# Performance work log

Hardware: AMD Instinct MI355X
Metric: run time of the kernel (lower is better)

Reference implementation:

```python
import jax, jax.numpy as jnp
import numpy as np

N, H, E, D, L = 100000, 20000, 1600000, 64, 3
F = 4 * D  # ffn hidden = out_dim * 4


def _ln(x, g, b, eps=1e-5):
    mu = x.mean(-1, keepdims=True)
    var = ((x - mu) ** 2).mean(-1, keepdims=True)
    return (x - mu) * jax.lax.rsqrt(var + eps) * g + b


def _gconv(x, W, b, src, dst, inv_sqrt_src, inv_sqrt_dst, n_dst):
    # DGL GraphConv, norm='both': D_dst^{-1/2} A D_src^{-1/2} (x W) + b
    h = (x * inv_sqrt_src[:, None]) @ W
    agg = jax.ops.segment_sum(h[src], dst, num_segments=n_dst)
    return agg * inv_sqrt_dst[:, None] + b


def setup_inputs() -> dict:
    key = jax.random.key(0)
    ks = jax.random.split(key, 24)
    s = 0.05
    inp = {
        'node_features': jax.random.normal(ks[0], (N, D), jnp.float32),
        'edge_src': jax.random.randint(ks[1], (E,), 0, N),
        'edge_dst': jax.random.randint(ks[2], (E,), 0, H),
        'n_hyper': H,
        # stacked per-layer params [L, ...]
        'Wn2h': jax.random.normal(ks[3], (L, D, D), jnp.float32) * s,
        'bn2h': jnp.zeros((L, D), jnp.float32),
        'Wh2n': jax.random.normal(ks[4], (L, D, D), jnp.float32) * s,
        'bh2n': jnp.zeros((L, D), jnp.float32),
        'W1': jax.random.normal(ks[5], (L, D, F), jnp.float32) * s,
        'b1': jnp.zeros((L, F), jnp.float32),
        'W2': jax.random.normal(ks[6], (L, F, D), jnp.float32) * s,
        'b2': jnp.zeros((L, D), jnp.float32),
        'g1': jnp.ones((L, D), jnp.float32),
        'be1': jnp.zeros((L, D), jnp.float32),
        'g2': jnp.ones((L, D), jnp.float32),
        'be2': jnp.zeros((L, D), jnp.float32),
        'gF': jnp.ones((D,), jnp.float32),
        'bF': jnp.zeros((D,), jnp.float32),
        'Wo': jax.random.normal(ks[7], (D, D), jnp.float32) * s,
        'bo': jnp.zeros((D,), jnp.float32),
    }
    return inp


def reference(node_features, edge_src, edge_dst, n_hyper, Wn2h, bn2h, Wh2n, bh2n,
              W1, b1, W2, b2, g1, be1, g2, be2, gF, bF, Wo, bo):
    n_nodes = node_features.shape[0]
    ones = jnp.ones(edge_src.shape[0], node_features.dtype)
    deg_node = jnp.clip(jax.ops.segment_sum(ones, edge_src, num_segments=n_nodes), 1.0)
    deg_hyp = jnp.clip(jax.ops.segment_sum(ones, edge_dst, num_segments=n_hyper), 1.0)
    is_node = jax.lax.rsqrt(deg_node)  # node out-degree^{-1/2}
    is_hyp = jax.lax.rsqrt(deg_hyp)    # hyperedge in-degree^{-1/2}

    def step(h, p):
        Wa, ba, Wb, bb, w1, c1, w2, c2, gg1, ee1, gg2, ee2 = p
        # node -> hyperedge conv (unused attention output is overwritten in the original)
        h_hyper = _gconv(h, Wa, ba, edge_src, edge_dst, is_node, is_hyp, n_hyper)
        # hyperedge -> node conv on reversed graph (degrees swap roles)
        h_node = _gconv(h_hyper, Wb, bb, edge_dst, edge_src, is_hyp, is_node, n_nodes)
        h = _ln(h + h_node, gg1, ee1)
        h_ffn = jax.nn.relu(h @ w1 + c1) @ w2 + c2
        h = _ln(h + h_ffn, gg2, ee2)
        return h, None

    h, _ = jax.lax.scan(step, node_features,
                        (Wn2h, bn2h, Wh2n, bh2n, W1, b1, W2, b2, g1, be1, g2, be2))
    h = _ln(h, gF, bF)
    return h @ Wo + bo
```

## Files before the change

kernel.cpp:

```cpp
#include <hip/hip_runtime.h>

#define HYP 20000
#define NLAYER 3
#define NB_H 313
#define NB_N 391
#define PT 4096

typedef __attribute__((ext_vector_type(8))) short short8;
typedef __attribute__((ext_vector_type(4))) float floatx4;

static __device__ __forceinline__ unsigned short f2bf(float f){
  union { float f; unsigned u; } v; v.f = f;
  unsigned r = v.u + 0x7FFF + ((v.u >> 16) & 1);
  return (unsigned short)(r >> 16);
}

__global__ __launch_bounds__(256) void k_hist(const int* __restrict__ src,
    const int* __restrict__ dst, int E, int* __restrict__ bh, int* __restrict__ bn){
  __shared__ int lh[NB_H + NB_N];
  int tid = threadIdx.x;
  for (int i = tid; i < NB_H + NB_N; i += 256) lh[i] = 0;
  __syncthreads();
  for (int i = blockIdx.x*256 + tid; i < E; i += gridDim.x*256){
    atomicAdd(&lh[dst[i] >> 6], 1);
    atomicAdd(&lh[NB_H + (src[i] >> 8)], 1);
  }
  __syncthreads();
  for (int i = tid; i < NB_H; i += 256) if (lh[i]) atomicAdd(&bh[i], lh[i]);
  for (int i = tid; i < NB_N; i += 256) if (lh[NB_H+i]) atomicAdd(&bn[i], lh[NB_H+i]);
}

__global__ __launch_bounds__(256) void k_bscan(const int* __restrict__ bh,
    const int* __restrict__ bn, int* __restrict__ bstart_h, int* __restrict__ gcur_h,
    int* __restrict__ bstart_n, int* __restrict__ gcur_n){
  __shared__ int ssc[4];
  __shared__ int scarry;
  int tid = threadIdx.x, lane = tid & 63, wv = tid >> 6;
  if (tid == 0) scarry = 0;
  __syncthreads();
  for (int base = 0; base < NB_H; base += 256){
    int i = base + tid; int v = (i < NB_H) ? bh[i] : 0; int x = v;
    #pragma unroll
    for (int o = 1; o < 64; o <<= 1){ int t = __shfl_up(x,o,64); if (lane >= o) x += t; }
    if (lane == 63) ssc[wv] = x;
    __syncthreads();
    int add = (wv>0?ssc[0]:0)+(wv>1?ssc[1]:0)+(wv>2?ssc[2]:0);
    int c = scarry;
    if (i < NB_H){ int ex = c + add + x - v; bstart_h[i] = ex; gcur_h[i] = ex; }
    __syncthreads();
    if (tid == 255) scarry = c + ssc[0]+ssc[1]+ssc[2]+ssc[3];
    __syncthreads();
  }
  if (tid == 0){ bstart_h[NB_H] = scarry; scarry = 0; }
  __syncthreads();
  for (int base = 0; base < NB_N; base += 256){
    int i = base + tid; int v = (i < NB_N) ? bn[i] : 0; int x = v;
    #pragma unroll
    for (int o = 1; o < 64; o <<= 1){ int t = __shfl_up(x,o,64); if (lane >= o) x += t; }
    if (lane == 63) ssc[wv] = x;
    __syncthreads();
    int add = (wv>0?ssc[0]:0)+(wv>1?ssc[1]:0)+(wv>2?ssc[2]:0);
    int c = scarry;
    if (i < NB_N){ int ex = c + add + x - v; bstart_n[i] = ex; gcur_n[i] = ex; }
    __syncthreads();
    if (tid == 255) scarry = c + ssc[0]+ssc[1]+ssc[2]+ssc[3];
    __syncthreads();
  }
  if (tid == 0) bstart_n[NB_N] = scarry;
}

__global__ __launch_bounds__(256) void k_partition(const int* __restrict__ keys,
    const int* __restrict__ pays, int E, int keyshift, int nb,
    int* __restrict__ gcur, unsigned* __restrict__ Ebuf){
  __shared__ unsigned sst[PT];
  __shared__ int lh[NB_N], lpre[NB_N], gb[NB_N];
  __shared__ int ssc[4];
  __shared__ int scarry;
  int tid = threadIdx.x, lane = tid & 63, wv = tid >> 6;
  int base = blockIdx.x*PT;
  int m = min(PT, E - base);
  for (int i = tid; i < nb; i += 256) lh[i] = 0;
  if (tid == 0) scarry = 0;
  __syncthreads();
  unsigned en[16]; int rk[16];
  #pragma unroll
  for (int j = 0; j < 16; ++j){
    int i = base + j*256 + tid;
    if (i < E){
      unsigned k = (unsigned)keys[i], p = (unsigned)pays[i];
      en[j] = (k << keyshift) | p;
      rk[j] = atomicAdd(&lh[en[j] >> 23], 1);
    } else { en[j] = 0; rk[j] = -1; }
  }
  __syncthreads();
  for (int b2 = 0; b2 < nb; b2 += 256){
    int i = b2 + tid; int v = (i < nb) ? lh[i] : 0; int x = v;
    #pragma unroll
    for (int o = 1; o < 64; o <<= 1){ int t = __shfl_up(x,o,64); if (lane >= o) x += t; }
    if (lane == 63) ssc[wv] = x;
    __syncthreads();
    int add = (wv>0?ssc[0]:0)+(wv>1?ssc[1]:0)+(wv>2?ssc[2]:0);
    int c = scarry;
    if (i < nb) lpre[i] = c + add + x - v;
    __syncthreads();
    if (tid == 255) scarry = c + ssc[0]+ssc[1]+ssc[2]+ssc[3];
    __syncthreads();
  }
  for (int i = tid; i < nb; i += 256) gb[i] = atomicAdd(&gcur[i], lh[i]);
  #pragma unroll
  for (int j = 0; j < 16; ++j){
    if (rk[j] >= 0){
      int bk = en[j] >> 23;
      sst[lpre[bk] + rk[j]] = en[j];
    }
  }
  __syncthreads();
  for (int j = tid; j < m; j += 256){
    unsigned e = sst[j];
    int bk = e >> 23;
    Ebuf[gb[bk] + (j - lpre[bk])] = e;
  }
}

__global__ __launch_bounds__(256) void k_build(const unsigned* __restrict__ Ebuf,
    const int* __restrict__ bstart, int keyshift, int ipb, int paymask, int limit,
    int* __restrict__ off, float* __restrict__ isv, int* __restrict__ csr){
  __shared__ int lcnt[256], lpre2[256], lcur[256];
  int tid = threadIdx.x, lane = tid & 63, wv = tid >> 6;
  int b = blockIdx.x;
  int base = bstart[b], m = bstart[b+1] - base;
  for (int i = tid; i < ipb; i += 256) lcnt[i] = 0;
  __syncthreads();
  for (int i = tid; i < m; i += 256){
    unsigned e = Ebuf[base + i];
    atomicAdd(&lcnt[(e >> keyshift) & (ipb-1)], 1);
  }
  __syncthreads();
  if (wv == 0){
    int carry = 0;
    for (int c = 0; c < ipb; c += 64){
      int li = c + lane;
      int v = lcnt[li]; int x = v;
      #pragma unroll
      for (int o = 1; o < 64; o <<= 1){ int t = __shfl_up(x,o,64); if (lane >= o) x += t; }
      int ex = carry + x - v;
      int id = b*ipb + li;
      if (id <= limit) off[id] = base + ex;
      if (id < limit) isv[id] = rsqrtf((float)(v > 0 ? v : 1));
      lpre2[li] = ex;
      carry += __shfl(x, 63, 64);
    }
  }
  for (int i = tid; i < ipb; i += 256) lcur[i] = 0;
  __syncthreads();
  for (int i = tid; i < m; i += 256){
    unsigned e = Ebuf[base + i];
    int li = (e >> keyshift) & (ipb-1);
    int pos = base + lpre2[li] + atomicAdd(&lcur[li], 1);
    csr[pos] = (int)(e & (unsigned)paymask);
  }
}

__global__ void k_prescale(const float* __restrict__ x, const float* __restrict__ isn,
                           unsigned short* __restrict__ xb, int nrows){
  int i = blockIdx.x*blockDim.x + threadIdx.x;
  int st = gridDim.x*blockDim.x;
  int tot = nrows*8;
  for (; i < tot; i += st){
    float s = isn[i >> 3];
    float4 v0 = *(const float4*)&x[(size_t)i*8];
    float4 v1 = *(const float4*)&x[(size_t)i*8 + 4];
    uint4 o;
    o.x = (unsigned)f2bf(v0.x*s) | ((unsigned)f2bf(v0.y*s) << 16);
    o.y = (unsigned)f2bf(v0.z*s) | ((unsigned)f2bf(v0.w*s) << 16);
    o.z = (unsigned)f2bf(v1.x*s) | ((unsigned)f2bf(v1.y*s) << 16);
    o.w = (unsigned)f2bf(v1.z*s) | ((unsigned)f2bf(v1.w*s) << 16);
    *(uint4*)&xb[(size_t)i*8] = o;
  }
}

__global__ void k_cvtall(const float* __restrict__ W1, const float* __restrict__ W2,
                         const float* __restrict__ Wa, const float* __restrict__ Wb,
                         const float* __restrict__ Wo,
                         unsigned short* __restrict__ W1T, unsigned short* __restrict__ W2T,
                         unsigned short* __restrict__ WaT, unsigned short* __restrict__ WbT,
                         unsigned short* __restrict__ WoT){
  int st = gridDim.x*blockDim.x;
  int t0 = blockIdx.x*blockDim.x + threadIdx.x;
  for (int j = t0; j < NLAYER*16384; j += st){
    int l = j >> 14, n = (j >> 6) & 255, k = j & 63;
    W1T[j] = f2bf(W1[l*16384 + k*256 + n]);
  }
  for (int j = t0; j < NLAYER*16384; j += st){
    int l = j >> 14, o = (j >> 8) & 63, kk = j & 255;
    W2T[j] = f2bf(W2[l*16384 + kk*64 + o]);
  }
  for (int j = t0; j < NLAYER*4096; j += st){
    int l = j >> 12, n = (j >> 6) & 63, k = j & 63;
    WaT[j] = f2bf(Wa[l*4096 + k*64 + n]);
  }
  for (int j = t0; j < NLAYER*4096; j += st){
    int l = j >> 12, n = (j >> 6) & 63, k = j & 63;
    WbT[j] = f2bf(Wb[l*4096 + k*64 + n]);
  }
  for (int j = t0; j < 4096; j += st){
    int n = (j >> 6) & 63, k = j & 63;
    WoT[j] = f2bf(Wo[k*64 + n]);
  }
}

template<int LSTR>
static __device__ __forceinline__ void stage64(const unsigned short* __restrict__ gsrc,
    unsigned short* __restrict__ ldst, int tid, int rows){
  int nch = rows*8;
  for (int idx = tid; idx < nch; idx += 256){
    int row = idx >> 3, kc = (idx & 7)*8;
    uint4 v = *(const uint4*)&gsrc[row*64 + kc];
    *(uint4*)&ldst[row*LSTR + kc] = v;
  }
}

static __device__ __forceinline__ void stage_swz(const unsigned short* __restrict__ g,
    int gs, unsigned short* __restrict__ l, int tid){
  #pragma unroll
  for (int it = 0; it < 2; ++it){
    int c = it*256 + tid;
    int row = c >> 3, s = c & 7;
    uint4 v = *(const uint4*)&g[row*gs + s*8];
    *(uint4*)&l[(row << 6) + ((((unsigned)(s ^ row)) & 7u) << 3)] = v;
  }
}

static __device__ __forceinline__ short8 rdswz(const unsigned short* __restrict__ l,
    int row, int slot){
  return *(const short8*)&l[(row << 6) + ((((unsigned)(slot ^ row)) & 7u) << 3)];
}

#define ACC8(u) \
  a0 += __uint_as_float(u.x << 16); a1 += __uint_as_float(u.x & 0xFFFF0000u); \
  a2 += __uint_as_float(u.y << 16); a3 += __uint_as_float(u.y & 0xFFFF0000u); \
  a4 += __uint_as_float(u.z << 16); a5 += __uint_as_float(u.z & 0xFFFF0000u); \
  a6 += __uint_as_float(u.w << 16); a7 += __uint_as_float(u.w & 0xFFFF0000u);

__global__ __launch_bounds__(256) void k_gather8(const unsigned short* __restrict__ feat,
    const int* __restrict__ csr, const int* __restrict__ off,
    unsigned short* __restrict__ agg, int nrows){
  int lane = threadIdx.x & 63, wvi = threadIdx.x >> 6;
  int g = lane >> 3;
  int ch = (lane & 7) * 8;
  int r = blockIdx.x*4 + wvi, stride = gridDim.x*4;
  for (; r < nrows; r += stride){
    int b = off[r], e = off[r+1];
    float a0=0,a1=0,a2=0,a3=0,a4=0,a5=0,a6=0,a7=0;
    int t = b;
    for (; t + 32 <= e; t += 32){
      int s0 = csr[t + g];
      int s1 = csr[t + 8 + g];
      int s2 = csr[t + 16 + g];
      int s3 = csr[t + 24 + g];
      uint4 u0 = *(const uint4*)&feat[(size_t)s0*64 + ch];
      uint4 u1 = *(const uint4*)&feat[(size_t)s1*64 + ch];
      uint4 u2 = *(const uint4*)&feat[(size_t)s2*64 + ch];
      uint4 u3 = *(const uint4*)&feat[(size_t)s3*64 + ch];
      ACC8(u0); ACC8(u1); ACC8(u2); ACC8(u3);
    }
    for (; t + 16 <= e; t += 16){
      int s0 = csr[t + g];
      int s1 = csr[t + 8 + g];
      uint4 u0 = *(const uint4*)&feat[(size_t)s0*64 + ch];
      uint4 u1 = *(const uint4*)&feat[(size_t)s1*64 + ch];
      ACC8(u0); ACC8(u1);
    }
    for (; t < e; t += 8){
      int idx = t + g;
      bool valid = idx < e;
      int s = csr[valid ? idx : b];
      uint4 u = *(const uint4*)&feat[(size_t)s*64 + ch];
      if (!valid){ u.x = 0; u.y = 0; u.z = 0; u.w = 0; }
      ACC8(u);
    }
    #pragma unroll
    for (int o = 8; o <= 32; o <<= 1){
      a0 += __shfl_xor(a0,o,64); a1 += __shfl_xor(a1,o,64);
      a2 += __shfl_xor(a2,o,64); a3 += __shfl_xor(a3,o,64);
      a4 += __shfl_xor(a4,o,64); a5 += __shfl_xor(a5,o,64);
      a6 += __shfl_xor(a6,o,64); a7 += __shfl_xor(a7,o,64);
    }
    if (g == 0){
      uint4 w;
      w.x = (unsigned)f2bf(a0) | ((unsigned)f2bf(a1) << 16);
      w.y = (unsigned)f2bf(a2) | ((unsigned)f2bf(a3) << 16);
      w.z = (unsigned)f2bf(a4) | ((unsigned)f2bf(a5) << 16);
      w.w = (unsigned)f2bf(a6) | ((unsigned)f2bf(a7) << 16);
      *(uint4*)&agg[(size_t)r*64 + ch] = w;
    }
  }
}

__global__ __launch_bounds__(64) void k_mmA(const unsigned short* __restrict__ aggb,
    const unsigned short* __restrict__ WaT, const float* __restrict__ bias,
    const float* __restrict__ ihy, unsigned short* __restrict__ ouths, int nrows){
  __shared__ unsigned short sWb[64*72];
  int lane = threadIdx.x;
  int quad = lane >> 4, n16 = lane & 15;
  for (int idx = lane; idx < 512; idx += 64){
    int row = idx >> 3, kc = (idx & 7)*8;
    *(uint4*)&sWb[row*72 + kc] = *(const uint4*)&WaT[row*64 + kc];
  }
  __syncthreads();
  int rowbase = blockIdx.x*16;
  int arow = min(rowbase + n16, nrows-1);
  short8 a0 = *(const short8*)&aggb[(size_t)arow*64 + quad*8];
  short8 a1 = *(const short8*)&aggb[(size_t)arow*64 + 32 + quad*8];
  float ih[4];
  #pragma unroll
  for (int r = 0; r < 4; ++r) ih[r] = ihy[min(rowbase + quad*4 + r, nrows-1)];
  #pragma unroll
  for (int ot = 0; ot < 4; ++ot){
    floatx4 c = (floatx4){0.f,0.f,0.f,0.f};
    short8 b0 = *(const short8*)&sWb[(ot*16+n16)*72 + quad*8];
    short8 b1 = *(const short8*)&sWb[(ot*16+n16)*72 + 32 + quad*8];
    c = __builtin_amdgcn_mfma_f32_16x16x32_bf16(a0, b0, c, 0, 0, 0);
    c = __builtin_amdgcn_mfma_f32_16x16x32_bf16(a1, b1, c, 0, 0, 0);
    float bl = bias[ot*16 + n16];
    #pragma unroll
    for (int r = 0; r < 4; ++r){
      int rr = rowbase + quad*4 + r;
      if (rr < nrows)
        ouths[(size_t)rr*64 + ot*16 + n16] = f2bf(fmaf(c[r], ih[r], bl) * ih[r]);
    }
  }
}

__global__ __launch_bounds__(256, 6) void k_fused(
    const unsigned short* __restrict__ aggb,
    const unsigned short* __restrict__ WbT,
    const float* __restrict__ bbg,
    const float* __restrict__ isn,
    const float* __restrict__ hin,
    const float* __restrict__ g1v, const float* __restrict__ be1v,
    const unsigned short* __restrict__ W1T, const float* __restrict__ b1g,
    const unsigned short* __restrict__ W2T, const float* __restrict__ b2g,
    const float* __restrict__ g2v, const float* __restrict__ be2v,
    float* __restrict__ Outp, unsigned short* __restrict__ Qs, int nrows)
{
  __shared__ unsigned short sA[64*64];
  __shared__ unsigned short sB[64*64];
  __shared__ unsigned short sPH[4*16*72];
  int tid = threadIdx.x;
  int lane = tid & 63, w = tid >> 6;
  int quad = lane >> 4, n16 = lane & 15;
  int rb = blockIdx.x*64 + w*16;

  stage_swz(WbT, 64, sA, tid);
  __syncthreads();

  float pP[4][4];
  float isr[4];
  {
    int arow = min(rb + n16, nrows-1);
    short8 a0 = *(const short8*)&aggb[(size_t)arow*64 + quad*8];
    short8 a1 = *(const short8*)&aggb[(size_t)arow*64 + 32 + quad*8];
    #pragma unroll
    for (int r = 0; r < 4; ++r) isr[r] = isn[min(rb + quad*4 + r, nrows-1)];
    #pragma unroll
    for (int ot = 0; ot < 4; ++ot){
      floatx4 c = (floatx4){0.f,0.f,0.f,0.f};
      short8 b0 = rdswz(sA, ot*16+n16, quad);
      short8 b1 = rdswz(sA, ot*16+n16, 4+quad);
      c = __builtin_amdgcn_mfma_f32_16x16x32_bf16(a0, b0, c, 0, 0, 0);
      c = __builtin_amdgcn_mfma_f32_16x16x32_bf16(a1, b1, c, 0, 0, 0);
      float bb = bbg[ot*16 + n16];
      #pragma unroll
      for (int r = 0; r < 4; ++r){
        int rr = min(rb + quad*4 + r, nrows-1);
        pP[ot][r] = fmaf(c[r], isr[r], bb) + hin[(size_t)rr*64 + ot*16 + n16];
      }
    }
  }
  {
    float gl[4], bl[4];
    #pragma unroll
    for (int ot = 0; ot < 4; ++ot){ gl[ot] = g1v[ot*16+n16]; bl[ot] = be1v[ot*16+n16]; }
    #pragma unroll
    for (int r = 0; r < 4; ++r){
      float sv = (pP[0][r] + pP[1][r]) + (pP[2][r] + pP[3][r]);
      float q = fmaf(pP[0][r], pP[0][r], pP[1][r]*pP[1][r]) +
                fmaf(pP[2][r], pP[2][r], pP[3][r]*pP[3][r]);
      #pragma unroll
      for (int o = 8; o >= 1; o >>= 1){
        sv += __shfl_xor(sv, o, 64);
        q  += __shfl_xor(q, o, 64);
      }
      float mu = sv*(1.f/64.f);
      float var = fmaf(-mu, mu, q*(1.f/64.f));
      float rs = rsqrtf(var + 1e-5f);
      #pragma unroll
      for (int ot = 0; ot < 4; ++ot)
        pP[ot][r] = fmaf((pP[ot][r]-mu)*rs, gl[ot], bl[ot]);
    }
  }
  unsigned short* myP = &sPH[w*16*72];
  #pragma unroll
  for (int ot = 0; ot < 4; ++ot)
    #pragma unroll
    for (int r = 0; r < 4; ++r)
      myP[(quad*4 + r)*72 + ot*16 + n16] = f2bf(pP[ot][r]);
  short8 p0 = *(const short8*)&myP[n16*72 + quad*8];
  short8 p1 = *(const short8*)&myP[n16*72 + 32 + quad*8];

  floatx4 acc2[4];
  #pragma unroll
  for (int t = 0; t < 4; ++t) acc2[t] = (floatx4){0.f,0.f,0.f,0.f};
  unsigned short* myHc = myP;

  for (int q = 0; q < 4; ++q){
    __syncthreads();
    stage_swz(W1T + q*64*64, 64, sA, tid);
    stage_swz(W2T + q*64, 256, sB, tid);
    __syncthreads();

    #pragma unroll
    for (int ck2 = 0; ck2 < 2; ++ck2){
      #pragma unroll
      for (int nt = 0; nt < 2; ++nt){
        int nl = ck2*32 + nt*16 + n16;
        floatx4 c = (floatx4){0.f,0.f,0.f,0.f};
        short8 b0 = rdswz(sA, nl, quad);
        short8 b1f = rdswz(sA, nl, 4+quad);
        c = __builtin_amdgcn_mfma_f32_16x16x32_bf16(p0, b0, c, 0, 0, 0);
        c = __builtin_amdgcn_mfma_f32_16x16x32_bf16(p1, b1f, c, 0, 0, 0);
        float bb = b1g[q*64 + nl];
        #pragma unroll
        for (int r = 0; r < 4; ++r){
          float h = fmaxf(c[r] + bb, 0.f);
          myHc[(quad*4 + r)*40 + nt*16 + n16] = f2bf(h);
        }
      }
      short8 a2 = *(const short8*)&myHc[n16*40 + quad*8];
      #pragma unroll
      for (int ot = 0; ot < 4; ++ot){
        short8 b2f = rdswz(sB, ot*16+n16, ck2*4 + quad);
        acc2[ot] = __builtin_amdgcn_mfma_f32_16x16x32_bf16(a2, b2f, acc2[ot], 0, 0, 0);
      }
    }
  }

  {
    float gl[4], bel[4];
    #pragma unroll
    for (int ot = 0; ot < 4; ++ot){ gl[ot] = g2v[ot*16 + n16]; bel[ot] = be2v[ot*16 + n16]; }
    float pre[4][4];
    #pragma unroll
    for (int ot = 0; ot < 4; ++ot){
      float b2c = b2g[ot*16 + n16];
      #pragma unroll
      for (int r = 0; r < 4; ++r)
        pre[ot][r] = acc2[ot][r] + b2c + pP[ot][r];
    }
    #pragma unroll
    for (int r = 0; r < 4; ++r){
      float sv = (pre[0][r] + pre[1][r]) + (pre[2][r] + pre[3][r]);
      float q = fmaf(pre[0][r], pre[0][r], pre[1][r]*pre[1][r]) +
                fmaf(pre[2][r], pre[2][r], pre[3][r]*pre[3][r]);
      #pragma unroll
      for (int o = 8; o >= 1; o >>= 1){
        sv += __shfl_xor(sv, o, 64);
        q  += __shfl_xor(q, o, 64);
      }
      float mu = sv*(1.f/64.f);
      float var = fmaf(-mu, mu, q*(1.f/64.f));
      float rs = rsqrtf(var + 1e-5f);
      int rr = rb + quad*4 + r;
      if (rr < nrows){
        float isr2 = isn[rr];
        #pragma unroll
        for (int ot = 0; ot < 4; ++ot){
          float ov = fmaf((pre[ot][r]-mu)*rs, gl[ot], bel[ot]);
          Outp[(size_t)rr*64 + ot*16 + n16] = ov;
          Qs[(size_t)rr*64 + ot*16 + n16] = f2bf(ov * isr2);
        }
      }
    }
  }
}

__global__ __launch_bounds__(256) void k_final(const float* __restrict__ Q,
    const unsigned short* __restrict__ WoT, const float* __restrict__ bog,
    const float* __restrict__ gF, const float* __restrict__ bF,
    float* __restrict__ out, int nrows){
  __shared__ unsigned short sWb[64*72];
  int tid = threadIdx.x;
  int lane = tid & 63, w = tid >> 6;
  int quad = lane >> 4, n16 = lane & 15;
  stage64<72>(WoT, sWb, tid, 64);
  __syncthreads();
  int rowbase = blockIdx.x*64 + w*16;
  int arow = min(rowbase + n16, nrows-1);
  float4 q0 = *(const float4*)&Q[(size_t)arow*64 + quad*8];
  float4 q1 = *(const float4*)&Q[(size_t)arow*64 + quad*8 + 4];
  float4 q2 = *(const float4*)&Q[(size_t)arow*64 + 32 + quad*8];
  float4 q3 = *(const float4*)&Q[(size_t)arow*64 + 32 + quad*8 + 4];
  float s = (q0.x+q0.y+q0.z+q0.w) + (q1.x+q1.y+q1.z+q1.w)
          + (q2.x+q2.y+q2.z+q2.w) + (q3.x+q3.y+q3.z+q3.w);
  float qq = (q0.x*q0.x+q0.y*q0.y+q0.z*q0.z+q0.w*q0.w)
           + (q1.x*q1.x+q1.y*q1.y+q1.z*q1.z+q1.w*q1.w)
           + (q2.x*q2.x+q2.y*q2.y+q2.z*q2.z+q2.w*q2.w)
           + (q3.x*q3.x+q3.y*q3.y+q3.z*q3.z+q3.w*q3.w);
  s += __shfl_xor(s, 16, 64);  qq += __shfl_xor(qq, 16, 64);
  s += __shfl_xor(s, 32, 64);  qq += __shfl_xor(qq, 32, 64);
  float mu = s*(1.f/64.f);
  float var = fmaf(-mu, mu, qq*(1.f/64.f));
  float rs = rsqrtf(var + 1e-5f);
  float4 g0 = *(const float4*)&gF[quad*8];
  float4 g1 = *(const float4*)&gF[quad*8 + 4];
  float4 g2 = *(const float4*)&gF[32 + quad*8];
  float4 g3 = *(const float4*)&gF[32 + quad*8 + 4];
  float4 f0 = *(const float4*)&bF[quad*8];
  float4 f1 = *(const float4*)&bF[quad*8 + 4];
  float4 f2 = *(const float4*)&bF[32 + quad*8];
  float4 f3 = *(const float4*)&bF[32 + quad*8 + 4];
  short8 a0, a1;
  a0[0]=f2bf(fmaf((q0.x-mu)*rs, g0.x, f0.x)); a0[1]=f2bf(fmaf((q0.y-mu)*rs, g0.y, f0.y));
  a0[2]=f2bf(fmaf((q0.z-mu)*rs, g0.z, f0.z)); a0[3]=f2bf(fmaf((q0.w-mu)*rs, g0.w, f0.w));
  a0[4]=f2bf(fmaf((q1.x-mu)*rs, g1.x, f1.x)); a0[5]=f2bf(fmaf((q1.y-mu)*rs, g1.y, f1.y));
  a0[6]=f2bf(fmaf((q1.z-mu)*rs, g1.z, f1.z)); a0[7]=f2bf(fmaf((q1.w-mu)*rs, g1.w, f1.w));
  a1[0]=f2bf(fmaf((q2.x-mu)*rs, g2.x, f2.x)); a1[1]=f2bf(fmaf((q2.y-mu)*rs, g2.y, f2.y));
  a1[2]=f2bf(fmaf((q2.z-mu)*rs, g2.z, f2.z)); a1[3]=f2bf(fmaf((q2.w-mu)*rs, g2.w, f2.w));
  a1[4]=f2bf(fmaf((q3.x-mu)*rs, g3.x, f3.x)); a1[5]=f2bf(fmaf((q3.y-mu)*rs, g3.y, f3.y));
  a1[6]=f2bf(fmaf((q3.z-mu)*rs, g3.z, f3.z)); a1[7]=f2bf(fmaf((q3.w-mu)*rs, g3.w, f3.w));
  #pragma unroll
  for (int ot = 0; ot < 4; ++ot){
    floatx4 c = (floatx4){0.f,0.f,0.f,0.f};
    short8 b0 = *(const short8*)&sWb[(ot*16+n16)*72 + quad*8];
    short8 b1 = *(const short8*)&sWb[(ot*16+n16)*72 + 32 + quad*8];
    c = __builtin_amdgcn_mfma_f32_16x16x32_bf16(a0, b0, c, 0, 0, 0);
    c = __builtin_amdgcn_mfma_f32_16x16x32_bf16(a1, b1, c, 0, 0, 0);
    float bol = bog[ot*16 + n16];
    #pragma unroll
    for (int r = 0; r < 4; ++r){
      int rr = rowbase + quad*4 + r;
      if (rr < nrows) out[(size_t)rr*64 + ot*16 + n16] = c[r] + bol;
    }
  }
}

extern "C" void kernel_launch(void* const* d_in, const int* in_sizes, int n_in,
                              void* d_out, int out_size, void* d_ws, size_t ws_size,
                              hipStream_t stream){
  const float* nf   = (const float*)d_in[0];
  const int*   esrc = (const int*)d_in[1];
  const int*   edst = (const int*)d_in[2];
  const float* Wn2h = (const float*)d_in[4];
  const float* bn2h = (const float*)d_in[5];
  const float* Wh2n = (const float*)d_in[6];
  const float* bh2n = (const float*)d_in[7];
  const float* W1   = (const float*)d_in[8];
  const float* b1   = (const float*)d_in[9];
  const float* W2   = (const float*)d_in[10];
  const float* b2   = (const float*)d_in[11];
  const float* g1   = (const float*)d_in[12];
  const float* be1  = (const float*)d_in[13];
  const float* g2   = (const float*)d_in[14];
  const float* be2  = (const float*)d_in[15];
  const float* gF   = (const float*)d_in[16];
  const float* bF   = (const float*)d_in[17];
  const float* Wo   = (const float*)d_in[18];
  const float* bo   = (const float*)d_in[19];
  const int N = in_sizes[0] / 64;
  const int E = in_sizes[1];
  const int H = HYP;
  float* out = (float*)d_out;

  char* w = (char*)d_ws;
  auto carve = [&](size_t bytes) -> char* {
    char* p = w; w += (bytes + 255) & ~(size_t)255; return p;
  };
  int* bh = (int*)carve((size_t)(NB_H + NB_N)*4);
  int* bn = bh + NB_H;
  int* bstart_h = (int*)carve((size_t)(NB_H+1)*4);
  int* gcur_h   = (int*)carve((size_t)NB_H*4);
  int* bstart_n = (int*)carve((size_t)(NB_N+1)*4);
  int* gcur_n   = (int*)carve((size_t)NB_N*4);
  unsigned* Ebuf_h = (unsigned*)carve((size_t)E*4);
  unsigned* Ebuf_n = (unsigned*)carve((size_t)E*4);
  int*   off_h = (int*)carve((size_t)(H+1)*4);
  int*   off_n = (int*)carve((size_t)(N+1)*4);
  float* is_h  = (float*)carve((size_t)H*4);
  float* is_n  = (float*)carve((size_t)N*4);
  int*   csr_h = (int*)carve((size_t)E*4);
  int*   csr_n = (int*)carve((size_t)E*4);
  unsigned short* aggxb = (unsigned short*)carve((size_t)H*64*2);
  unsigned short* agghb = (unsigned short*)carve((size_t)N*64*2);
  float* Qb    = (float*)carve((size_t)N*64*4);
  unsigned short* hhsb = (unsigned short*)carve((size_t)H*64*2);
  unsigned short* xb0  = (unsigned short*)carve((size_t)N*64*2);
  unsigned short* Qs   = (unsigned short*)carve((size_t)N*64*2);
  unsigned short* W1g16 = (unsigned short*)carve((size_t)NLAYER*64*256*2);
  unsigned short* W2g16 = (unsigned short*)carve((size_t)NLAYER*256*64*2);
  unsigned short* Wag16 = (unsigned short*)carve((size_t)NLAYER*4096*2);
  unsigned short* Wbg16 = (unsigned short*)carve((size_t)NLAYER*4096*2);
  unsigned short* Wog16 = (unsigned short*)carve((size_t)4096*2);

  hipMemsetAsync(bh, 0, (size_t)(NB_H + NB_N)*4, stream);
  k_cvtall<<<96, 256, 0, stream>>>(W1, W2, Wn2h, Wh2n, Wo,
                                   W1g16, W2g16, Wag16, Wbg16, Wog16);
  k_hist<<<512, 256, 0, stream>>>(esrc, edst, E, bh, bn);
  k_bscan<<<1, 256, 0, stream>>>(bh, bn, bstart_h, gcur_h, bstart_n, gcur_n);
  k_partition<<<(E + PT - 1)/PT, 256, 0, stream>>>(edst, esrc, E, 17, NB_H, gcur_h, Ebuf_h);
  k_partition<<<(E + PT - 1)/PT, 256, 0, stream>>>(esrc, edst, E, 15, NB_N, gcur_n, Ebuf_n);
  k_build<<<NB_H, 256, 0, stream>>>(Ebuf_h, bstart_h, 17, 64, 0x1FFFF, H, off_h, is_h, csr_h);
  k_build<<<NB_N, 256, 0, stream>>>(Ebuf_n, bstart_n, 15, 256, 0x7FFF, N, off_n, is_n, csr_n);
  k_prescale<<<2048, 256, 0, stream>>>(nf, is_n, xb0, N);

  const int NB64 = (N + 63)/64;
  const int HB16 = (H + 15)/16;
  for (int l = 0; l < NLAYER; ++l){
    const float* hin = (l == 0) ? nf : Qb;
    const unsigned short* hsrc = (l == 0) ? xb0 : Qs;
    k_gather8<<<2048, 256, 0, stream>>>(hsrc, csr_h, off_h, aggxb, H);
    k_mmA<<<HB16, 64, 0, stream>>>(aggxb, Wag16 + l*4096, bn2h + l*64, is_h, hhsb, H);
    k_gather8<<<2048, 256, 0, stream>>>(hhsb, csr_n, off_n, agghb, N);
    k_fused<<<NB64, 256, 0, stream>>>(agghb, Wbg16 + l*4096, bh2n + l*64, is_n, hin,
                                      g1 + l*64, be1 + l*64,
                                      W1g16 + l*64*256, b1 + l*256,
                                      W2g16 + l*256*64, b2 + l*64,
                                      g2 + l*64, be2 + l*64, Qb, Qs, N);
  }
  k_final<<<NB64, 256, 0, stream>>>(Qb, Wog16, bo, gF, bF, out, N);
}
```

Measured before the change: 534.9 us.

## Read MFMA weight operands directly from global memory instead of LDS staging

Removes LDS staging of weight matrices in k_mmA, k_fused and k_final, so MFMA B operands are loaded straight from global memory, where the small weights should stay cache-resident. This drops the per-block staging loops and block-wide barriers, including the four barrier pairs per FFN chunk in k_fused, and cuts LDS use so more blocks can be resident. The launch-bounds occupancy hint on k_fused is also removed. The cost is more global/L2 load traffic and latency on each MFMA operand fetch, with no reuse across the waves of a block.

After: 624.6 us. 16.8% more time.

```diff
diff --git a/kernel.cpp b/kernel.cpp
--- a/kernel.cpp
+++ b/kernel.cpp
@@ -207,33 +207,6 @@
     int n = (j >> 6) & 63, k = j & 63;
     WoT[j] = f2bf(Wo[k*64 + n]);
   }
-}
-
-template<int LSTR>
-static __device__ __forceinline__ void stage64(const unsigned short* __restrict__ gsrc,
-    unsigned short* __restrict__ ldst, int tid, int rows){
-  int nch = rows*8;
-  for (int idx = tid; idx < nch; idx += 256){
-    int row = idx >> 3, kc = (idx & 7)*8;
-    uint4 v = *(const uint4*)&gsrc[row*64 + kc];
-    *(uint4*)&ldst[row*LSTR + kc] = v;
-  }
-}
-
-static __device__ __forceinline__ void stage_swz(const unsigned short* __restrict__ g,
-    int gs, unsigned short* __restrict__ l, int tid){
-  #pragma unroll
-  for (int it = 0; it < 2; ++it){
-    int c = it*256 + tid;
-    int row = c >> 3, s = c & 7;
-    uint4 v = *(const uint4*)&g[row*gs + s*8];
-    *(uint4*)&l[(row << 6) + ((((unsigned)(s ^ row)) & 7u) << 3)] = v;
-  }
-}
-
-static __device__ __forceinline__ short8 rdswz(const unsigned short* __restrict__ l,
-    int row, int slot){
-  return *(const short8*)&l[(row << 6) + ((((unsigned)(slot ^ row)) & 7u) << 3)];
 }
 
 #define ACC8(u) \
@@ -300,14 +273,8 @@
 __global__ __launch_bounds__(64) void k_mmA(const unsigned short* __restrict__ aggb,
     const unsigned short* __restrict__ WaT, const float* __restrict__ bias,
     const float* __restrict__ ihy, unsigned short* __restrict__ ouths, int nrows){
-  __shared__ unsigned short sWb[64*72];
-  int lane = threadIdx.x;
+  int lane = threadIdx.x & 63;
   int quad = lane >> 4, n16 = lane & 15;
-  for (int idx = lane; idx < 512; idx += 64){
-    int row = idx >> 3, kc = (idx & 7)*8;
-    *(uint4*)&sWb[row*72 + kc] = *(const uint4*)&WaT[row*64 + kc];
-  }
-  __syncthreads();
   int rowbase = blockIdx.x*16;
   int arow = min(rowbase + n16, nrows-1);
   short8 a0 = *(const short8*)&aggb[(size_t)arow*64 + quad*8];
@@ -318,8 +285,8 @@
   #pragma unroll
   for (int ot = 0; ot < 4; ++ot){
     floatx4 c = (floatx4){0.f,0.f,0.f,0.f};
-    short8 b0 = *(const short8*)&sWb[(ot*16+n16)*72 + quad*8];
-    short8 b1 = *(const short8*)&sWb[(ot*16+n16)*72 + 32 + quad*8];
+    short8 b0 = *(const short8*)&WaT[(ot*16+n16)*64 + quad*8];
+    short8 b1 = *(const short8*)&WaT[(ot*16+n16)*64 + 32 + quad*8];
     c = __builtin_amdgcn_mfma_f32_16x16x32_bf16(a0, b0, c, 0, 0, 0);
     c = __builtin_amdgcn_mfma_f32_16x16x32_bf16(a1, b1, c, 0, 0, 0);
     float bl = bias[ot*16 + n16];
@@ -332,7 +299,7 @@
   }
 }
 
-__global__ __launch_bounds__(256, 6) void k_fused(
+__global__ __launch_bounds__(256) void k_fused(
     const unsigned short* __restrict__ aggb,
     const unsigned short* __restrict__ WbT,
     const float* __restrict__ bbg,
@@ -344,38 +311,33 @@
     const float* __restrict__ g2v, const float* __restrict__ be2v,
     float* __restrict__ Outp, unsigned short* __restrict__ Qs, int nrows)
 {
-  __shared__ unsigned short sA[64*64];
-  __shared__ unsigned short sB[64*64];
   __shared__ unsigned short sPH[4*16*72];
   int tid = threadIdx.x;
   int lane = tid & 63, w = tid >> 6;
   int quad = lane >> 4, n16 = lane & 15;
   int rb = blockIdx.x*64 + w*16;
-
-  stage_swz(WbT, 64, sA, tid);
-  __syncthreads();
+  unsigned short* myP = &sPH[w*16*72];
+
+  int arow = min(rb + n16, nrows-1);
+  short8 a0 = *(const short8*)&aggb[(size_t)arow*64 + quad*8];
+  short8 a1 = *(const short8*)&aggb[(size_t)arow*64 + 32 + quad*8];
 
   float pP[4][4];
   float isr[4];
-  {
-    int arow = min(rb + n16, nrows-1);
-    short8 a0 = *(const short8*)&aggb[(size_t)arow*64 + quad*8];
-    short8 a1 = *(const short8*)&aggb[(size_t)arow*64 + 32 + quad*8];
-    #pragma unroll
-    for (int r = 0; r < 4; ++r) isr[r] = isn[min(rb + quad*4 + r, nrows-1)];
-    #pragma unroll
-    for (int ot = 0; ot < 4; ++ot){
-      floatx4 c = (floatx4){0.f,0.f,0.f,0.f};
-      short8 b0 = rdswz(sA, ot*16+n16, quad);
-      short8 b1 = rdswz(sA, ot*16+n16, 4+quad);
-      c = __builtin_amdgcn_mfma_f32_16x16x32_bf16(a0, b0, c, 0, 0, 0);
-      c = __builtin_amdgcn_mfma_f32_16x16x32_bf16(a1, b1, c, 0, 0, 0);
-      float bb = bbg[ot*16 + n16];
-      #pragma unroll
-      for (int r = 0; r < 4; ++r){
-        int rr = min(rb + quad*4 + r, nrows-1);
-        pP[ot][r] = fmaf(c[r], isr[r], bb) + hin[(size_t)rr*64 + ot*16 + n16];
-      }
+  #pragma unroll
+  for (int r = 0; r < 4; ++r) isr[r] = isn[min(rb + quad*4 + r, nrows-1)];
+  #pragma unroll
+  for (int ot = 0; ot < 4; ++ot){
+    floatx4 c = (floatx4){0.f,0.f,0.f,0.f};
+    short8 b0 = *(const short8*)&WbT[(ot*16+n16)*64 + quad*8];
+    short8 b1 = *(const short8*)&WbT[(ot*16+n16)*64 + 32 + quad*8];
+    c = __builtin_amdgcn_mfma_f32_16x16x32_bf16(a0, b0, c, 0, 0, 0);
+    c = __builtin_amdgcn_mfma_f32_16x16x32_bf16(a1, b1, c, 0, 0, 0);
+    float bb = bbg[ot*16 + n16];
+    #pragma unroll
+    for (int r = 0; r < 4; ++r){
+      int rr = min(rb + quad*4 + r, nrows-1);
+      pP[ot][r] = fmaf(c[r], isr[r], bb) + hin[(size_t)rr*64 + ot*16 + n16];
     }
   }
   {
@@ -400,7 +362,6 @@
         pP[ot][r] = fmaf((pP[ot][r]-mu)*rs, gl[ot], bl[ot]);
     }
   }
-  unsigned short* myP = &sPH[w*16*72];
   #pragma unroll
   for (int ot = 0; ot < 4; ++ot)
     #pragma unroll
@@ -412,35 +373,30 @@
   floatx4 acc2[4];
   #pragma unroll
   for (int t = 0; t < 4; ++t) acc2[t] = (floatx4){0.f,0.f,0.f,0.f};
-  unsigned short* myHc = myP;
-
+
+  #pragma unroll
   for (int q = 0; q < 4; ++q){
-    __syncthreads();
-    stage_swz(W1T + q*64*64, 64, sA, tid);
-    stage_swz(W2T + q*64, 256, sB, tid);
-    __syncthreads();
-
     #pragma unroll
     for (int ck2 = 0; ck2 < 2; ++ck2){
       #pragma unroll
       for (int nt = 0; nt < 2; ++nt){
-        int nl = ck2*32 + nt*16 + n16;
+        int nn = q*64 + ck2*32 + nt*16 + n16;
         floatx4 c = (floatx4){0.f,0.f,0.f,0.f};
-        short8 b0 = rdswz(sA, nl, quad);
-        short8 b1f = rdswz(sA, nl, 4+quad);
+        short8 b0 = *(const short8*)&W1T[nn*64 + quad*8];
+        short8 b1f = *(const short8*)&W1T[nn*64 + 32 + quad*8];
         c = __builtin_amdgcn_mfma_f32_16x16x32_bf16(p0, b0, c, 0, 0, 0);
         c = __builtin_amdgcn_mfma_f32_16x16x32_bf16(p1, b1f, c, 0, 0, 0);
-        float bb = b1g[q*64 + nl];
+        float bb = b1g[nn];
         #pragma unroll
         for (int r = 0; r < 4; ++r){
           float h = fmaxf(c[r] + bb, 0.f);
-          myHc[(quad*4 + r)*40 + nt*16 + n16] = f2bf(h);
+          myP[(quad*4 + r)*40 + nt*16 + n16] = f2bf(h);
         }
       }
-      short8 a2 = *(const short8*)&myHc[n16*40 + quad*8];
+      short8 a2 = *(const short8*)&myP[n16*40 + quad*8];
       #pragma unroll
       for (int ot = 0; ot < 4; ++ot){
-        short8 b2f = rdswz(sB, ot*16+n16, ck2*4 + quad);
+        short8 b2f = *(const short8*)&W2T[(ot*16+n16)*256 + q*64 + ck2*32 + quad*8];
         acc2[ot] = __builtin_amdgcn_mfma_f32_16x16x32_bf16(a2, b2f, acc2[ot], 0, 0, 0);
       }
     }
@@ -489,12 +445,9 @@
     const unsigned short* __restrict__ WoT, const float* __restrict__ bog,
     const float* __restrict__ gF, const float* __restrict__ bF,
     float* __restrict__ out, int nrows){
-  __shared__ unsigned short sWb[64*72];
   int tid = threadIdx.x;
   int lane = tid & 63, w = tid >> 6;
   int quad = lane >> 4, n16 = lane & 15;
-  stage64<72>(WoT, sWb, tid, 64);
-  __syncthreads();
   int rowbase = blockIdx.x*64 + w*16;
   int arow = min(rowbase + n16, nrows-1);
   float4 q0 = *(const float4*)&Q[(size_t)arow*64 + quad*8];
@@ -532,8 +485,8 @@
   #pragma unroll
   for (int ot = 0; ot < 4; ++ot){
     floatx4 c = (floatx4){0.f,0.f,0.f,0.f};
-    short8 b0 = *(const short8*)&sWb[(ot*16+n16)*72 + quad*8];
-    short8 b1 = *(const short8*)&sWb[(ot*16+n16)*72 + 32 + quad*8];
+    short8 b0 = *(const short8*)&WoT[(ot*16+n16)*64 + quad*8];
+    short8 b1 = *(const short8*)&WoT[(ot*16+n16)*64 + 32 + quad*8];
     c = __builtin_amdgcn_mfma_f32_16x16x32_bf16(a0, b0, c, 0, 0, 0);
     c = __builtin_amdgcn_mfma_f32_16x16x32_bf16(a1, b1, c, 0, 0, 0);
     float bol = bog[ot*16 + n16];
```

## Fuse hyperedge-to-node gather into the fused node-update kernel

Applied to the files above, without the earlier changes.

Removes the separate k_gather8 launch for the hyperedge-to-node aggregation. k_fused now gathers the CSR neighbours itself, one wave per 16 rows, reduces across lanes with shuffles, and writes the bf16 aggregate straight into shared memory for the MFMA. This avoids writing and re-reading the N x 64 aggregate buffer and saves one kernel launch per layer. In exchange, occupancy drops because the launch_bounds min-blocks hint was removed, and the gather loop processes rows serially within each wave, which may hide latency less well than the standalone gather kernel.

Result: slower. 571.3 us (+6.8%).

```diff
diff --git a/kernel.cpp b/kernel.cpp
--- a/kernel.cpp
+++ b/kernel.cpp
@@ -332,8 +332,10 @@
   }
 }
 
-__global__ __launch_bounds__(256, 6) void k_fused(
-    const unsigned short* __restrict__ aggb,
+__global__ __launch_bounds__(256) void k_fused(
+    const unsigned short* __restrict__ feat,
+    const int* __restrict__ csr,
+    const int* __restrict__ off,
     const unsigned short* __restrict__ WbT,
     const float* __restrict__ bbg,
     const float* __restrict__ isn,
@@ -351,31 +353,82 @@
   int lane = tid & 63, w = tid >> 6;
   int quad = lane >> 4, n16 = lane & 15;
   int rb = blockIdx.x*64 + w*16;
+  unsigned short* myP = &sPH[w*16*72];
 
   stage_swz(WbT, 64, sA, tid);
-  __syncthreads();
+
+  {
+    int g = lane >> 3;
+    int ch = (lane & 7) * 8;
+    for (int r16 = 0; r16 < 16; ++r16){
+      int row = min(rb + r16, nrows-1);
+      int b = off[row], e = off[row+1];
+      float a0=0,a1=0,a2=0,a3=0,a4=0,a5=0,a6=0,a7=0;
+      int t = b;
+      for (; t + 32 <= e; t += 32){
+        int s0 = csr[t + g];
+        int s1 = csr[t + 8 + g];
+        int s2 = csr[t + 16 + g];
+        int s3 = csr[t + 24 + g];
+        uint4 u0 = *(const uint4*)&feat[(size_t)s0*64 + ch];
+        uint4 u1 = *(const uint4*)&feat[(size_t)s1*64 + ch];
+        uint4 u2 = *(const uint4*)&feat[(size_t)s2*64 + ch];
+        uint4 u3 = *(const uint4*)&feat[(size_t)s3*64 + ch];
+        ACC8(u0); ACC8(u1); ACC8(u2); ACC8(u3);
+      }
+      for (; t + 16 <= e; t += 16){
+        int s0 = csr[t + g];
+        int s1 = csr[t + 8 + g];
+        uint4 u0 = *(const uint4*)&feat[(size_t)s0*64 + ch];
+        uint4 u1 = *(const uint4*)&feat[(size_t)s1*64 + ch];
+        ACC8(u0); ACC8(u1);
+      }
+      for (; t < e; t += 8){
+        int idx = t + g;
+        bool valid = idx < e;
+        int s = csr[valid ? idx : b];
+        uint4 u = *(const uint4*)&feat[(size_t)s*64 + ch];
+        if (!valid){ u.x = 0; u.y = 0; u.z = 0; u.w = 0; }
+        ACC8(u);
+      }
+      #pragma unroll
+      for (int o = 8; o <= 32; o <<= 1){
+        a0 += __shfl_xor(a0,o,64); a1 += __shfl_xor(a1,o,64);
+        a2 += __shfl_xor(a2,o,64); a3 += __shfl_xor(a3,o,64);
+        a4 += __shfl_xor(a4,o,64); a5 += __shfl_xor(a5,o,64);
+        a6 += __shfl_xor(a6,o,64); a7 += __shfl_xor(a7,o,64);
+      }
+      if (g == 0){
+        uint4 wv;
+        wv.x = (unsigned)f2bf(a0) | ((unsigned)f2bf(a1) << 16);
+        wv.y = (unsigned)f2bf(a2) | ((unsigned)f2bf(a3) << 16);
+        wv.z = (unsigned)f2bf(a4) | ((unsigned)f2bf(a5) << 16);
+        wv.w = (unsigned)f2bf(a6) | ((unsigned)f2bf(a7) << 16);
+        *(uint4*)&myP[r16*72 + ch] = wv;
+      }
+    }
+  }
+  __syncthreads();
+
+  short8 a0 = *(const short8*)&myP[n16*72 + quad*8];
+  short8 a1 = *(const short8*)&myP[n16*72 + 32 + quad*8];
 
   float pP[4][4];
   float isr[4];
-  {
-    int arow = min(rb + n16, nrows-1);
-    short8 a0 = *(const short8*)&aggb[(size_t)arow*64 + quad*8];
-    short8 a1 = *(const short8*)&aggb[(size_t)arow*64 + 32 + quad*8];
-    #pragma unroll
-    for (int r = 0; r < 4; ++r) isr[r] = isn[min(rb + quad*4 + r, nrows-1)];
-    #pragma unroll
-    for (int ot = 0; ot < 4; ++ot){
-      floatx4 c = (floatx4){0.f,0.f,0.f,0.f};
-      short8 b0 = rdswz(sA, ot*16+n16, quad);
-      short8 b1 = rdswz(sA, ot*16+n16, 4+quad);
-      c = __builtin_amdgcn_mfma_f32_16x16x32_bf16(a0, b0, c, 0, 0, 0);
-      c = __builtin_amdgcn_mfma_f32_16x16x32_bf16(a1, b1, c, 0, 0, 0);
-      float bb = bbg[ot*16 + n16];
-      #pragma unroll
-      for (int r = 0; r < 4; ++r){
-        int rr = min(rb + quad*4 + r, nrows-1);
-        pP[ot][r] = fmaf(c[r], isr[r], bb) + hin[(size_t)rr*64 + ot*16 + n16];
-      }
+  #pragma unroll
+  for (int r = 0; r < 4; ++r) isr[r] = isn[min(rb + quad*4 + r, nrows-1)];
+  #pragma unroll
+  for (int ot = 0; ot < 4; ++ot){
+    floatx4 c = (floatx4){0.f,0.f,0.f,0.f};
+    short8 b0 = rdswz(sA, ot*16+n16, quad);
+    short8 b1 = rdswz(sA, ot*16+n16, 4+quad);
+    c = __builtin_amdgcn_mfma_f32_16x16x32_bf16(a0, b0, c, 0, 0, 0);
+    c = __builtin_amdgcn_mfma_f32_16x16x32_bf16(a1, b1, c, 0, 0, 0);
+    float bb = bbg[ot*16 + n16];
+    #pragma unroll
+    for (int r = 0; r < 4; ++r){
+      int rr = min(rb + quad*4 + r, nrows-1);
+      pP[ot][r] = fmaf(c[r], isr[r], bb) + hin[(size_t)rr*64 + ot*16 + n16];
     }
   }
   {
@@ -400,7 +453,6 @@
         pP[ot][r] = fmaf((pP[ot][r]-mu)*rs, gl[ot], bl[ot]);
     }
   }
-  unsigned short* myP = &sPH[w*16*72];
   #pragma unroll
   for (int ot = 0; ot < 4; ++ot)
     #pragma unroll
@@ -591,7 +643,6 @@
   int*   csr_h = (int*)carve((size_t)E*4);
   int*   csr_n = (int*)carve((size_t)E*4);
   unsigned short* aggxb = (unsigned short*)carve((size_t)H*64*2);
-  unsigned short* agghb = (unsigned short*)carve((size_t)N*64*2);
   float* Qb    = (float*)carve((size_t)N*64*4);
   unsigned short* hhsb = (unsigned short*)carve((size_t)H*64*2);
   unsigned short* xb0  = (unsigned short*)carve((size_t)N*64*2);
@@ -620,8 +671,8 @@
     const unsigned short* hsrc = (l == 0) ? xb0 : Qs;
     k_gather8<<<2048, 256, 0, stream>>>(hsrc, csr_h, off_h, aggxb, H);
     k_mmA<<<HB16, 64, 0, stream>>>(aggxb, Wag16 + l*4096, bn2h + l*64, is_h, hhsb, H);
-    k_gather8<<<2048, 256, 0, stream>>>(hhsb, csr_n, off_n, agghb, N);
-    k_fused<<<NB64, 256, 0, stream>>>(agghb, Wbg16 + l*4096, bh2n + l*64, is_n, hin,
+    k_fused<<<NB64, 256, 0, stream>>>(hhsb, csr_n, off_n,
+                                      Wbg16 + l*4096, bh2n + l*64, is_n, hin,
                                       g1 + l*64, be1 + l*64,
                                       W1g16 + l*64*256, b1 + l*256,
                                       W2g16 + l*256*64, b2 + l*64,
```

## Make fused FFN kernel persistent with all weights resident in LDS

Applied to the files above, without the earlier changes.

The fused node-update kernel becomes persistent: 256 blocks of 512 threads stage the Wb, W1 and W2 bf16 weights plus the bias and LayerNorm vectors into LDS and registers once. Each wave then loops over 16-row groups with no block barriers inside the loop. This replaces restaging W1/W2 chunks with four pairs of __syncthreads for every 64 rows. In exchange, LDS use grows to about 90KB per block, which limits occupancy to roughly one block per CU and leaves less latency hiding for the hin and aggb loads.

Result: faster. 511.5 us (-4.4%).

```diff
diff --git a/kernel.cpp b/kernel.cpp
--- a/kernel.cpp
+++ b/kernel.cpp
@@ -220,15 +220,11 @@
   }
 }
 
-static __device__ __forceinline__ void stage_swz(const unsigned short* __restrict__ g,
+static __device__ __forceinline__ void stage_swz512(const unsigned short* __restrict__ g,
     int gs, unsigned short* __restrict__ l, int tid){
-  #pragma unroll
-  for (int it = 0; it < 2; ++it){
-    int c = it*256 + tid;
-    int row = c >> 3, s = c & 7;
-    uint4 v = *(const uint4*)&g[row*gs + s*8];
-    *(uint4*)&l[(row << 6) + ((((unsigned)(s ^ row)) & 7u) << 3)] = v;
-  }
+  int row = tid >> 3, s = tid & 7;
+  uint4 v = *(const uint4*)&g[row*gs + s*8];
+  *(uint4*)&l[(row << 6) + ((((unsigned)(s ^ row)) & 7u) << 3)] = v;
 }
 
 static __device__ __forceinline__ short8 rdswz(const unsigned short* __restrict__ l,
@@ -332,7 +328,7 @@
   }
 }
 
-__global__ __launch_bounds__(256, 6) void k_fused(
+__global__ __launch_bounds__(512) void k_fused(
     const unsigned short* __restrict__ aggb,
     const unsigned short* __restrict__ WbT,
     const float* __restrict__ bbg,
@@ -344,44 +340,66 @@
     const float* __restrict__ g2v, const float* __restrict__ be2v,
     float* __restrict__ Outp, unsigned short* __restrict__ Qs, int nrows)
 {
-  __shared__ unsigned short sA[64*64];
-  __shared__ unsigned short sB[64*64];
-  __shared__ unsigned short sPH[4*16*72];
+  __shared__ unsigned short sWb[64*64];
+  __shared__ unsigned short sW1[4*64*64];
+  __shared__ unsigned short sW2[4*64*64];
+  __shared__ unsigned short sPH[8*16*72];
   int tid = threadIdx.x;
   int lane = tid & 63, w = tid >> 6;
   int quad = lane >> 4, n16 = lane & 15;
-  int rb = blockIdx.x*64 + w*16;
-
-  stage_swz(WbT, 64, sA, tid);
-  __syncthreads();
-
-  float pP[4][4];
-  float isr[4];
-  {
+  unsigned short* myP = &sPH[w*16*72];
+
+  stage_swz512(WbT, 64, sWb, tid);
+  #pragma unroll
+  for (int q = 0; q < 4; ++q) stage_swz512(W1T + q*64*64, 64, sW1 + q*4096, tid);
+  #pragma unroll
+  for (int q = 0; q < 4; ++q) stage_swz512(W2T + q*64, 256, sW2 + q*4096, tid);
+
+  float bbv[4], g1l[4], be1l[4], b2v[4], g2l[4], be2l[4];
+  #pragma unroll
+  for (int ot = 0; ot < 4; ++ot){
+    bbv[ot] = bbg[ot*16 + n16];
+    g1l[ot] = g1v[ot*16 + n16];  be1l[ot] = be1v[ot*16 + n16];
+    b2v[ot] = b2g[ot*16 + n16];
+    g2l[ot] = g2v[ot*16 + n16];  be2l[ot] = be2v[ot*16 + n16];
+  }
+  float b1v[4][4];
+  #pragma unroll
+  for (int q = 0; q < 4; ++q)
+    #pragma unroll
+    for (int c2 = 0; c2 < 4; ++c2)
+      b1v[q][c2] = b1g[q*64 + c2*16 + n16];
+
+  __syncthreads();
+
+  int ngrp = (nrows + 15) >> 4;
+  int wwid = blockIdx.x*8 + w;
+  int nw = gridDim.x*8;
+
+  for (int grp = wwid; grp < ngrp; grp += nw){
+    int rb = grp*16;
+
     int arow = min(rb + n16, nrows-1);
     short8 a0 = *(const short8*)&aggb[(size_t)arow*64 + quad*8];
     short8 a1 = *(const short8*)&aggb[(size_t)arow*64 + 32 + quad*8];
+
+    float pP[4][4];
+    float isr[4];
     #pragma unroll
     for (int r = 0; r < 4; ++r) isr[r] = isn[min(rb + quad*4 + r, nrows-1)];
     #pragma unroll
     for (int ot = 0; ot < 4; ++ot){
       floatx4 c = (floatx4){0.f,0.f,0.f,0.f};
-      short8 b0 = rdswz(sA, ot*16+n16, quad);
-      short8 b1 = rdswz(sA, ot*16+n16, 4+quad);
+      short8 b0 = rdswz(sWb, ot*16+n16, quad);
+      short8 b1 = rdswz(sWb, ot*16+n16, 4+quad);
       c = __builtin_amdgcn_mfma_f32_16x16x32_bf16(a0, b0, c, 0, 0, 0);
       c = __builtin_amdgcn_mfma_f32_16x16x32_bf16(a1, b1, c, 0, 0, 0);
-      float bb = bbg[ot*16 + n16];
       #pragma unroll
       for (int r = 0; r < 4; ++r){
         int rr = min(rb + quad*4 + r, nrows-1);
-        pP[ot][r] = fmaf(c[r], isr[r], bb) + hin[(size_t)rr*64 + ot*16 + n16];
+        pP[ot][r] = fmaf(c[r], isr[r], bbv[ot]) + hin[(size_t)rr*64 + ot*16 + n16];
       }
     }
-  }
-  {
-    float gl[4], bl[4];
-    #pragma unroll
-    for (int ot = 0; ot < 4; ++ot){ gl[ot] = g1v[ot*16+n16]; bl[ot] = be1v[ot*16+n16]; }
     #pragma unroll
     for (int r = 0; r < 4; ++r){
       float sv = (pP[0][r] + pP[1][r]) + (pP[2][r] + pP[3][r]);
@@ -397,67 +415,56 @@
       float rs = rsqrtf(var + 1e-5f);
       #pragma unroll
       for (int ot = 0; ot < 4; ++ot)
-        pP[ot][r] = fmaf((pP[ot][r]-mu)*rs, gl[ot], bl[ot]);
-    }
-  }
-  unsigned short* myP = &sPH[w*16*72];
-  #pragma unroll
-  for (int ot = 0; ot < 4; ++ot)
-    #pragma unroll
-    for (int r = 0; r < 4; ++r)
-      myP[(quad*4 + r)*72 + ot*16 + n16] = f2bf(pP[ot][r]);
-  short8 p0 = *(const short8*)&myP[n16*72 + quad*8];
-  short8 p1 = *(const short8*)&myP[n16*72 + 32 + quad*8];
-
-  floatx4 acc2[4];
-  #pragma unroll
-  for (int t = 0; t < 4; ++t) acc2[t] = (floatx4){0.f,0.f,0.f,0.f};
-  unsigned short* myHc = myP;
-
-  for (int q = 0; q < 4; ++q){
-    __syncthreads();
-    stage_swz(W1T + q*64*64, 64, sA, tid);
-    stage_swz(W2T + q*64, 256, sB, tid);
-    __syncthreads();
-
-    #pragma unroll
-    for (int ck2 = 0; ck2 < 2; ++ck2){
-      #pragma unroll
-      for (int nt = 0; nt < 2; ++nt){
-        int nl = ck2*32 + nt*16 + n16;
-        floatx4 c = (floatx4){0.f,0.f,0.f,0.f};
-        short8 b0 = rdswz(sA, nl, quad);
-        short8 b1f = rdswz(sA, nl, 4+quad);
-        c = __builtin_amdgcn_mfma_f32_16x16x32_bf16(p0, b0, c, 0, 0, 0);
-        c = __builtin_amdgcn_mfma_f32_16x16x32_bf16(p1, b1f, c, 0, 0, 0);
-        float bb = b1g[q*64 + nl];
+        pP[ot][r] = fmaf((pP[ot][r]-mu)*rs, g1l[ot], be1l[ot]);
+    }
+    #pragma unroll
+    for (int ot = 0; ot < 4; ++ot)
+      #pragma unroll
+      for (int r = 0; r < 4; ++r)
+        myP[(quad*4 + r)*72 + ot*16 + n16] = f2bf(pP[ot][r]);
+    short8 p0 = *(const short8*)&myP[n16*72 + quad*8];
+    short8 p1 = *(const short8*)&myP[n16*72 + 32 + quad*8];
+
+    floatx4 acc2[4];
+    #pragma unroll
+    for (int t = 0; t < 4; ++t) acc2[t] = (floatx4){0.f,0.f,0.f,0.f};
+
+    #pragma unroll
+    for (int q = 0; q < 4; ++q){
+      const unsigned short* sA = sW1 + q*4096;
+      const unsigned short* sB = sW2 + q*4096;
+      #pragma unroll
+      for (int ck2 = 0; ck2 < 2; ++ck2){
         #pragma unroll
-        for (int r = 0; r < 4; ++r){
-          float h = fmaxf(c[r] + bb, 0.f);
-          myHc[(quad*4 + r)*40 + nt*16 + n16] = f2bf(h);
+        for (int nt = 0; nt < 2; ++nt){
+          int nl = ck2*32 + nt*16 + n16;
+          floatx4 c = (floatx4){0.f,0.f,0.f,0.f};
+          short8 b0 = rdswz(sA, nl, quad);
+          short8 b1f = rdswz(sA, nl, 4+quad);
+          c = __builtin_amdgcn_mfma_f32_16x16x32_bf16(p0, b0, c, 0, 0, 0);
+          c = __builtin_amdgcn_mfma_f32_16x16x32_bf16(p1, b1f, c, 0, 0, 0);
+          float bb = b1v[q][ck2*2 + nt];
+          #pragma unroll
+          for (int r = 0; r < 4; ++r){
+            float h = fmaxf(c[r] + bb, 0.f);
+            myP[(quad*4 + r)*40 + nt*16 + n16] = f2bf(h);
+          }
+        }
+        short8 a2 = *(const short8*)&myP[n16*40 + quad*8];
+        #pragma unroll
+        for (int ot = 0; ot < 4; ++ot){
+          short8 b2f = rdswz(sB, ot*16+n16, ck2*4 + quad);
+          acc2[ot] = __builtin_amdgcn_mfma_f32_16x16x32_bf16(a2, b2f, acc2[ot], 0, 0, 0);
         }
       }
-      short8 a2 = *(const short8*)&myHc[n16*40 + quad*8];
-      #pragma unroll
-      for (int ot = 0; ot < 4; ++ot){
-        short8 b2f = rdswz(sB, ot*16+n16, ck2*4 + quad);
-        acc2[ot] = __builtin_amdgcn_mfma_f32_16x16x32_bf16(a2, b2f, acc2[ot], 0, 0, 0);
-      }
-    }
-  }
-
-  {
-    float gl[4], bel[4];
-    #pragma unroll
-    for (int ot = 0; ot < 4; ++ot){ gl[ot] = g2v[ot*16 + n16]; bel[ot] = be2v[ot*16 + n16]; }
+    }
+
     float pre[4][4];
     #pragma unroll
-    for (int ot = 0; ot < 4; ++ot){
-      float b2c = b2g[ot*16 + n16];
+    for (int ot = 0; ot < 4; ++ot)
       #pragma unroll
       for (int r = 0; r < 4; ++r)
-        pre[ot][r] = acc2[ot][r] + b2c + pP[ot][r];
-    }
+        pre[ot][r] = acc2[ot][r] + b2v[ot] + pP[ot][r];
     #pragma unroll
     for (int r = 0; r < 4; ++r){
       float sv = (pre[0][r] + pre[1][r]) + (pre[2][r] + pre[3][r]);
@@ -476,7 +483,7 @@
         float isr2 = isn[rr];
         #pragma unroll
         for (int ot = 0; ot < 4; ++ot){
-          float ov = fmaf((pre[ot][r]-mu)*rs, gl[ot], bel[ot]);
+          float ov = fmaf((pre[ot][r]-mu)*rs, g2l[ot], be2l[ot]);
           Outp[(size_t)rr*64 + ot*16 + n16] = ov;
           Qs[(size_t)rr*64 + ot*16 + n16] = f2bf(ov * isr2);
         }
@@ -621,11 +628,11 @@
     k_gather8<<<2048, 256, 0, stream>>>(hsrc, csr_h, off_h, aggxb, H);
     k_mmA<<<HB16, 64, 0, stream>>>(aggxb, Wag16 + l*4096, bn2h + l*64, is_h, hhsb, H);
     k_gather8<<<2048, 256, 0, stream>>>(hhsb, csr_n, off_n, agghb, N);
-    k_fused<<<NB64, 256, 0, stream>>>(agghb, Wbg16 + l*4096, bh2n + l*64, is_n, hin,
-                                      g1 + l*64, be1 + l*64,
-                                      W1g16 + l*64*256, b1 + l*256,
-                                      W2g16 + l*256*64, b2 + l*64,
-                                      g2 + l*64, be2 + l*64, Qb, Qs, N);
+    k_fused<<<256, 512, 0, stream>>>(agghb, Wbg16 + l*4096, bh2n + l*64, is_n, hin,
+                                     g1 + l*64, be1 + l*64,
+                                     W1g16 + l*64*256, b1 + l*256,
+                                     W2g16 + l*256*64, b2 + l*64,
+                                     g2 + l*64, be2 + l*64, Qb, Qs, N);
   }
   k_final<<<NB64, 256, 0, stream>>>(Qb, Wog16, bo, gF, bF, out, N);
 }
```
